# Performance work log

Measured on AMD Instinct MI355X. Metric: run time of the kernel, lower is better.

The kernel has to match this reference:

```python
import jax, jax.numpy as jnp
import numpy as np

E = 8      # n_rm_states
D = 256    # flattened input dim
H = 64     # hidden width (hard-coded in module)
A = 18     # n_actions
B = 65536  # batch


def setup_inputs() -> dict:
    key = jax.random.key(0)
    ks = jax.random.split(key, 16)
    s = lambda k, shape, fan_in: jax.random.normal(k, shape, jnp.float32) * (1.0 / np.sqrt(fan_in))
    inp = {
        "state": jax.random.normal(ks[0], (B, D), jnp.float32),
        "rm_state": jax.random.randint(ks[1], (B,), 0, E),
        # stacked per-expert params: layer i weight [E, in, out], bias [E, out]
        "W1": s(ks[2], (E, D, H), D), "b1": jnp.zeros((E, H), jnp.float32),
        "W2": s(ks[3], (E, H, H), H), "b2": jnp.zeros((E, H), jnp.float32),
        "W3": s(ks[4], (E, H, H), H), "b3": jnp.zeros((E, H), jnp.float32),
        "W4": s(ks[5], (E, H, H), H), "b4": jnp.zeros((E, H), jnp.float32),
        "W5": s(ks[6], (E, H, H), H), "b5": jnp.zeros((E, H), jnp.float32),
        "W6": s(ks[7], (E, H, A), H), "b6": jnp.zeros((E, A), jnp.float32),
    }
    return inp


def reference(state, rm_state, W1, b1, W2, b2, W3, b3, W4, b4, W5, b5, W6, b6):
    x = state.reshape(state.shape[0], -1)              # [B, D]
    # Run all E expert MLPs densely over the batch, then select per-row expert.
    h = jax.nn.relu(jnp.einsum('bd,edh->ebh', x, W1) + b1[:, None, :])   # [E, B, H]
    h = jax.nn.relu(jnp.einsum('ebh,ehk->ebk', h, W2) + b2[:, None, :])
    h = jax.nn.relu(jnp.einsum('ebh,ehk->ebk', h, W3) + b3[:, None, :])
    h = jax.nn.relu(jnp.einsum('ebh,ehk->ebk', h, W4) + b4[:, None, :])
    h = jax.nn.relu(jnp.einsum('ebh,ehk->ebk', h, W5) + b5[:, None, :])
    out_all = jnp.einsum('ebh,eha->eba', h, W6) + b6[:, None, :]          # [E, B, A]
    # scatter-back: actions[b] = expert[rm_state[b]](x[b])
    actions = out_all[rm_state, jnp.arange(x.shape[0])]                    # [B, A]
    return actions
```

## Files before the change

### kernel.cpp

```cpp
#include <hip/hip_runtime.h>


#define NE   8
#define DIM  256
#define HID  64
#define NA   18

typedef __attribute__((ext_vector_type(8))) short short8;
typedef __attribute__((ext_vector_type(4))) float f32x4;
#define MFMA __builtin_amdgcn_mfma_f32_16x16x32_bf16

__device__ __forceinline__ unsigned short f2bf(float f) {
    unsigned u = __builtin_bit_cast(unsigned, f);
    u += 0x7fff + ((u >> 16) & 1);
    return (unsigned short)(u >> 16);
}
__device__ __forceinline__ float bf2f(unsigned short h) {
    unsigned u = ((unsigned)h) << 16;
    return __builtin_bit_cast(float, u);
}
__device__ __forceinline__ void split8(const float* xs, short8& hi, short8& lo) {
    #pragma unroll
    for (int j = 0; j < 8; ++j) {
        unsigned short h = f2bf(xs[j]);
        hi[j] = (short)h;
        lo[j] = (short)f2bf(xs[j] - bf2f(h));
    }
}

__global__ __launch_bounds__(256) void histo_kernel(const int* __restrict__ rm,
                                                    int* __restrict__ hist) {
    __shared__ int wc[4][NE];
    const int t = threadIdx.x, w = t >> 6, l = t & 63;
    const int e = rm[blockIdx.x * 256 + t];
    #pragma unroll
    for (int q = 0; q < NE; ++q) {
        unsigned long long m = __ballot(e == q);
        if (l == 0) wc[w][q] = __popcll(m);
    }
    __syncthreads();
    if (t < NE) hist[blockIdx.x * NE + t] = wc[0][t] + wc[1][t] + wc[2][t] + wc[3][t];
}

__global__ __launch_bounds__(256) void scan_kernel(const int* __restrict__ hist,
                                                   int* __restrict__ base,
                                                   int* __restrict__ meta) {
    __shared__ int s[256][NE];
    __shared__ int tot[NE];
    const int t = threadIdx.x;
    int v[NE], own[NE];
    #pragma unroll
    for (int e = 0; e < NE; ++e) { own[e] = hist[t * NE + e]; v[e] = own[e]; }
    for (int off = 1; off < 256; off <<= 1) {
        #pragma unroll
        for (int e = 0; e < NE; ++e) s[t][e] = v[e];
        __syncthreads();
        if (t >= off) {
            #pragma unroll
            for (int e = 0; e < NE; ++e) v[e] += s[t - off][e];
        }
        __syncthreads();
    }
    if (t == 255) {
        #pragma unroll
        for (int e = 0; e < NE; ++e) tot[e] = v[e];
    }
    __syncthreads();
    int es[NE + 1]; es[0] = 0;
    #pragma unroll
    for (int e = 0; e < NE; ++e) es[e + 1] = es[e] + tot[e];
    #pragma unroll
    for (int e = 0; e < NE; ++e) base[t * NE + e] = es[e] + v[e] - own[e];
    if (t == 0) {
        #pragma unroll
        for (int e = 0; e < NE; ++e) meta[e] = tot[e];
        #pragma unroll
        for (int e = 0; e <= NE; ++e) meta[8 + e] = es[e];
        int ts = 0; meta[17] = 0;
        #pragma unroll
        for (int e = 0; e < NE; ++e) { ts += (tot[e] + 63) >> 6; meta[17 + e + 1] = ts; }
    }
}

__global__ __launch_bounds__(256) void scatter_kernel(const int* __restrict__ rm,
                                                      const int* __restrict__ base,
                                                      int* __restrict__ perm) {
    __shared__ int wc[4][NE];
    __shared__ int wb[4][NE];
    const int t = threadIdx.x, w = t >> 6, l = t & 63;
    const int i = blockIdx.x * 256 + t;
    const int e = rm[i];
    const unsigned long long ltm = (1ull << l) - 1ull;
    int rank = 0;
    #pragma unroll
    for (int q = 0; q < NE; ++q) {
        unsigned long long m = __ballot(e == q);
        if (e == q) rank = __popcll(m & ltm);
        if (l == 0) wc[w][q] = __popcll(m);
    }
    __syncthreads();
    if (t < 32) {
        int ww = t >> 3, q = t & 7;
        int b = base[blockIdx.x * NE + q];
        for (int p = 0; p < ww; ++p) b += wc[p][q];
        wb[ww][q] = b;
    }
    __syncthreads();
    perm[wb[w][e] + rank] = i;
}

__global__ __launch_bounds__(256) void prep_kernel(
    const float* __restrict__ W1, const float* __restrict__ W2,
    const float* __restrict__ W3, const float* __restrict__ W4,
    const float* __restrict__ W5, const float* __restrict__ W6,
    short* __restrict__ W1H, short* __restrict__ W1L,
    short* __restrict__ W2H, short* __restrict__ W2L,
    short* __restrict__ W3H, short* __restrict__ W3L,
    short* __restrict__ W4H, short* __restrict__ W4L,
    short* __restrict__ W5H, short* __restrict__ W5L,
    short* __restrict__ W6H, short* __restrict__ W6L) {
    const int idx = blockIdx.x * 256 + threadIdx.x;
    float v; short* H; short* L; int sidx;
    if (idx < 131072) {
        int e = idx >> 14, r = idx & 16383;
        int ks = r >> 11, nt = (r >> 9) & 3, l = (r >> 3) & 63, j = r & 7;
        int k = ks * 32 + ((l >> 4) << 3) + j, n = (nt << 4) + (l & 15);
        v = W1[(e * DIM + k) * HID + n];
        H = W1H; L = W1L; sidx = idx;
    } else if (idx < 131072 + 4 * 32768) {
        int layer = (idx - 131072) >> 15;
        int local = (idx - 131072) & 32767;
        int e = local >> 12, r = local & 4095;
        int ks = r >> 11, nt = (r >> 9) & 3, l = (r >> 3) & 63, j = r & 7;
        int k = ks * 32 + ((l >> 4) << 3) + j, n = (nt << 4) + (l & 15);
        const float* W = (layer == 0) ? W2 : (layer == 1) ? W3 : (layer == 2) ? W4 : W5;
        v = W[(e * HID + k) * HID + n];
        H = (layer == 0) ? W2H : (layer == 1) ? W3H : (layer == 2) ? W4H : W5H;
        L = (layer == 0) ? W2L : (layer == 1) ? W3L : (layer == 2) ? W4L : W5L;
        sidx = local;
    } else if (idx < 131072 + 4 * 32768 + 16384) {
        int local = idx - (131072 + 4 * 32768);
        int e = local >> 11, r = local & 2047;
        int ks = r >> 10, nt = (r >> 9) & 1, l = (r >> 3) & 63, j = r & 7;
        int k = ks * 32 + ((l >> 4) << 3) + j, n = (nt << 4) + (l & 15);
        v = (n < NA) ? W6[(e * HID + k) * NA + n] : 0.0f;
        H = W6H; L = W6L; sidx = local;
    } else return;
    unsigned short h = f2bf(v);
    H[sidx] = (short)h;
    L[sidx] = (short)f2bf(v - bf2f(h));
}

template <int NT>
__device__ __forceinline__ void gemm_k64(const float* hsrc, int l,
                                         const short* __restrict__ WH,
                                         const short* __restrict__ WL,
                                         f32x4* acc) {
    const int lg = l >> 4, lr = l & 15;
    #pragma unroll
    for (int ks = 0; ks < 2; ++ks) {
        const float* ap = hsrc + lr * 68 + ks * 32 + lg * 8;
        float4 v0 = *(const float4*)(ap);
        float4 v1 = *(const float4*)(ap + 4);
        float xs[8] = {v0.x, v0.y, v0.z, v0.w, v1.x, v1.y, v1.z, v1.w};
        short8 ahi, alo; split8(xs, ahi, alo);
        #pragma unroll
        for (int nt = 0; nt < NT; ++nt) {
            const short8 bhi = *(const short8*)(WH + ((ks * NT + nt) * 64 + l) * 8);
            const short8 blo = *(const short8*)(WL + ((ks * NT + nt) * 64 + l) * 8);
            acc[nt] = MFMA(ahi, bhi, acc[nt], 0, 0, 0);
            acc[nt] = MFMA(alo, bhi, acc[nt], 0, 0, 0);
            acc[nt] = MFMA(ahi, blo, acc[nt], 0, 0, 0);
        }
    }
}

template <int NT, bool RELU>
__device__ __forceinline__ void finish_to_lds(float* hdst, int l,
                                              const float* __restrict__ bias,
                                              f32x4* acc) {
    const int lg = l >> 4, lr = l & 15;
    #pragma unroll
    for (int nt = 0; nt < NT; ++nt) {
        float bv = bias[nt * 16 + lr];
        #pragma unroll
        for (int r = 0; r < 4; ++r) {
            float v = acc[nt][r] + bv;
            if (RELU) v = fmaxf(v, 0.0f);
            hdst[(lg * 4 + r) * 68 + nt * 16 + lr] = v;
        }
    }
}

__global__ __launch_bounds__(256) void mlp_mfma(
    const float* __restrict__ x, const int* __restrict__ perm,
    const int* __restrict__ meta,
    const short* __restrict__ W1H, const short* __restrict__ W1L,
    const short* __restrict__ W2H, const short* __restrict__ W2L,
    const short* __restrict__ W3H, const short* __restrict__ W3L,
    const short* __restrict__ W4H, const short* __restrict__ W4L,
    const short* __restrict__ W5H, const short* __restrict__ W5L,
    const short* __restrict__ W6H, const short* __restrict__ W6L,
    const float* __restrict__ b1, const float* __restrict__ b2,
    const float* __restrict__ b3, const float* __restrict__ b4,
    const float* __restrict__ b5, const float* __restrict__ b6,
    float* __restrict__ out) {
    __shared__ __align__(16) float hbuf[4][16][68];
    const int blk = blockIdx.x;
    if (blk >= meta[17 + NE]) return;
    int e = 0;
    #pragma unroll 1
    while (blk >= meta[17 + e + 1]) ++e;
    const int lt = blk - meta[17 + e];
    const int cnt = meta[e];
    const int pbase = meta[8 + e];
    const int t = threadIdx.x, w = t >> 6, l = t & 63;
    const int lg = l >> 4, lr = l & 15;
    const int li = lt * 64 + w * 16 + lr;
    const int row = perm[pbase + min(li, cnt - 1)];
    float* hw = &hbuf[w][0][0];
    const f32x4 zero = {0.0f, 0.0f, 0.0f, 0.0f};

    {
        f32x4 acc[4] = {zero, zero, zero, zero};
        const float* xr = x + (size_t)row * DIM + lg * 8;
        const short* WHp = W1H + (size_t)e * 32 * 512 + l * 8;
        const short* WLp = W1L + (size_t)e * 32 * 512 + l * 8;
        #pragma unroll
        for (int ks = 0; ks < 8; ++ks) {
            float4 v0 = *(const float4*)(xr + ks * 32);
            float4 v1 = *(const float4*)(xr + ks * 32 + 4);
            float xs[8] = {v0.x, v0.y, v0.z, v0.w, v1.x, v1.y, v1.z, v1.w};
            short8 ahi, alo; split8(xs, ahi, alo);
            #pragma unroll
            for (int nt = 0; nt < 4; ++nt) {
                const short8 bhi = *(const short8*)(WHp + (ks * 4 + nt) * 512);
                const short8 blo = *(const short8*)(WLp + (ks * 4 + nt) * 512);
                acc[nt] = MFMA(ahi, bhi, acc[nt], 0, 0, 0);
                acc[nt] = MFMA(alo, bhi, acc[nt], 0, 0, 0);
                acc[nt] = MFMA(ahi, blo, acc[nt], 0, 0, 0);
            }
        }
        finish_to_lds<4, true>(hw, l, b1 + e * HID, acc);
    }
    {
        f32x4 acc[4] = {zero, zero, zero, zero};
        gemm_k64<4>(hw, l, W2H + e * 8 * 512, W2L + e * 8 * 512, acc);
        finish_to_lds<4, true>(hw, l, b2 + e * HID, acc);
    }
    {
        f32x4 acc[4] = {zero, zero, zero, zero};
        gemm_k64<4>(hw, l, W3H + e * 8 * 512, W3L + e * 8 * 512, acc);
        finish_to_lds<4, true>(hw, l, b3 + e * HID, acc);
    }
    {
        f32x4 acc[4] = {zero, zero, zero, zero};
        gemm_k64<4>(hw, l, W4H + e * 8 * 512, W4L + e * 8 * 512, acc);
        finish_to_lds<4, true>(hw, l, b4 + e * HID, acc);
    }
    {
        f32x4 acc[4] = {zero, zero, zero, zero};
        gemm_k64<4>(hw, l, W5H + e * 8 * 512, W5L + e * 8 * 512, acc);
        finish_to_lds<4, true>(hw, l, b5 + e * HID, acc);
    }
    {
        f32x4 acc[2] = {zero, zero};
        gemm_k64<2>(hw, l, W6H + e * 4 * 512, W6L + e * 4 * 512, acc);
        const float* b6p = b6 + e * NA;
        #pragma unroll
        for (int r = 0; r < 4; ++r) {
            const int drow = lg * 4 + r;
            const int rs = __shfl(row, drow, 64);
            const bool valid = (lt * 64 + w * 16 + drow) < cnt;
            #pragma unroll
            for (int nt = 0; nt < 2; ++nt) {
                const int col = nt * 16 + lr;
                if (valid && col < NA)
                    out[(size_t)rs * NA + col] = acc[nt][r] + b6p[col];
            }
        }
    }
}

extern "C" void kernel_launch(void* const* d_in, const int* in_sizes, int n_in,
                              void* d_out, int out_size, void* d_ws, size_t ws_size,
                              hipStream_t stream) {
    const float* x  = (const float*)d_in[0];
    const int*   rm = (const int*)d_in[1];
    const float* W1 = (const float*)d_in[2];   const float* b1 = (const float*)d_in[3];
    const float* W2 = (const float*)d_in[4];   const float* b2 = (const float*)d_in[5];
    const float* W3 = (const float*)d_in[6];   const float* b3 = (const float*)d_in[7];
    const float* W4 = (const float*)d_in[8];   const float* b4 = (const float*)d_in[9];
    const float* W5 = (const float*)d_in[10];  const float* b5 = (const float*)d_in[11];
    const float* W6 = (const float*)d_in[12];  const float* b6 = (const float*)d_in[13];
    float* out = (float*)d_out;

    const int B = in_sizes[1];
    const int nblk = B / 256;

    int* hist = (int*)d_ws;
    int* base = hist + nblk * NE;
    int* meta = base + nblk * NE;
    int* perm = meta + 32;
    short* W1H = (short*)(perm + B);
    short* W1L = W1H + 131072;
    short* W2H = W1L + 131072;  short* W2L = W2H + 32768;
    short* W3H = W2L + 32768;   short* W3L = W3H + 32768;
    short* W4H = W3L + 32768;   short* W4L = W4H + 32768;
    short* W5H = W4L + 32768;   short* W5L = W5H + 32768;
    short* W6H = W5L + 32768;   short* W6L = W6H + 16384;

    histo_kernel<<<nblk, 256, 0, stream>>>(rm, hist);
    scan_kernel<<<1, 256, 0, stream>>>(hist, base, meta);
    scatter_kernel<<<nblk, 256, 0, stream>>>(rm, base, perm);
    prep_kernel<<<1088, 256, 0, stream>>>(W1, W2, W3, W4, W5, W6,
                                          W1H, W1L, W2H, W2L, W3H, W3L,
                                          W4H, W4L, W5H, W5L, W6H, W6L);
    mlp_mfma<<<B / 64 + NE, 256, 0, stream>>>(x, perm, meta,
                                              W1H, W1L, W2H, W2L, W3H, W3L,
                                              W4H, W4L, W5H, W5L, W6H, W6L,
                                              b1, b2, b3, b4, b5, b6, out);
}
```

Before: 153.9 us.

## Fuse prep/histogram and scan/scatter kernels; split MFMA accumulators into three chains

Merges the weight-split prep and the routing histogram into one launch, and merges the single-block scan with the scatter. Each scatter block now redoes the full 256-block scan redundantly using wave shuffles. This cuts four small launches plus the serial scan kernel down to two. In the MLP, the three bf16x3 MFMA products go into separate accumulators so they no longer form one dependent chain, B fragments are loaded before the MFMAs, packed bf16 conversion intrinsics are used, and launch bounds add an occupancy hint. These changes add register pressure and redundant scan work per block.

```diff
diff --git a/kernel.cpp b/kernel.cpp
--- a/kernel.cpp
+++ b/kernel.cpp
@@ -1,4 +1,5 @@
 #include <hip/hip_runtime.h>
+#include <hip/hip_bf16.h>
 
 
 #define NE   8
@@ -19,97 +20,26 @@
     unsigned u = ((unsigned)h) << 16;
     return __builtin_bit_cast(float, u);
 }
-__device__ __forceinline__ void split8(const float* xs, short8& hi, short8& lo) {
-    #pragma unroll
-    for (int j = 0; j < 8; ++j) {
-        unsigned short h = f2bf(xs[j]);
-        hi[j] = (short)h;
-        lo[j] = (short)f2bf(xs[j] - bf2f(h));
-    }
-}
-
-__global__ __launch_bounds__(256) void histo_kernel(const int* __restrict__ rm,
-                                                    int* __restrict__ hist) {
-    __shared__ int wc[4][NE];
-    const int t = threadIdx.x, w = t >> 6, l = t & 63;
-    const int e = rm[blockIdx.x * 256 + t];
-    #pragma unroll
-    for (int q = 0; q < NE; ++q) {
-        unsigned long long m = __ballot(e == q);
-        if (l == 0) wc[w][q] = __popcll(m);
-    }
-    __syncthreads();
-    if (t < NE) hist[blockIdx.x * NE + t] = wc[0][t] + wc[1][t] + wc[2][t] + wc[3][t];
-}
-
-__global__ __launch_bounds__(256) void scan_kernel(const int* __restrict__ hist,
-                                                   int* __restrict__ base,
-                                                   int* __restrict__ meta) {
-    __shared__ int s[256][NE];
-    __shared__ int tot[NE];
-    const int t = threadIdx.x;
-    int v[NE], own[NE];
-    #pragma unroll
-    for (int e = 0; e < NE; ++e) { own[e] = hist[t * NE + e]; v[e] = own[e]; }
-    for (int off = 1; off < 256; off <<= 1) {
-        #pragma unroll
-        for (int e = 0; e < NE; ++e) s[t][e] = v[e];
-        __syncthreads();
-        if (t >= off) {
-            #pragma unroll
-            for (int e = 0; e < NE; ++e) v[e] += s[t - off][e];
-        }
-        __syncthreads();
-    }
-    if (t == 255) {
-        #pragma unroll
-        for (int e = 0; e < NE; ++e) tot[e] = v[e];
-    }
-    __syncthreads();
-    int es[NE + 1]; es[0] = 0;
-    #pragma unroll
-    for (int e = 0; e < NE; ++e) es[e + 1] = es[e] + tot[e];
-    #pragma unroll
-    for (int e = 0; e < NE; ++e) base[t * NE + e] = es[e] + v[e] - own[e];
-    if (t == 0) {
-        #pragma unroll
-        for (int e = 0; e < NE; ++e) meta[e] = tot[e];
-        #pragma unroll
-        for (int e = 0; e <= NE; ++e) meta[8 + e] = es[e];
-        int ts = 0; meta[17] = 0;
-        #pragma unroll
-        for (int e = 0; e < NE; ++e) { ts += (tot[e] + 63) >> 6; meta[17 + e + 1] = ts; }
-    }
-}
-
-__global__ __launch_bounds__(256) void scatter_kernel(const int* __restrict__ rm,
-                                                      const int* __restrict__ base,
-                                                      int* __restrict__ perm) {
-    __shared__ int wc[4][NE];
-    __shared__ int wb[4][NE];
-    const int t = threadIdx.x, w = t >> 6, l = t & 63;
-    const int i = blockIdx.x * 256 + t;
-    const int e = rm[i];
-    const unsigned long long ltm = (1ull << l) - 1ull;
-    int rank = 0;
-    #pragma unroll
-    for (int q = 0; q < NE; ++q) {
-        unsigned long long m = __ballot(e == q);
-        if (e == q) rank = __popcll(m & ltm);
-        if (l == 0) wc[w][q] = __popcll(m);
-    }
-    __syncthreads();
-    if (t < 32) {
-        int ww = t >> 3, q = t & 7;
-        int b = base[blockIdx.x * NE + q];
-        for (int p = 0; p < ww; ++p) b += wc[p][q];
-        wb[ww][q] = b;
-    }
-    __syncthreads();
-    perm[wb[w][e] + rank] = i;
-}
-
-__global__ __launch_bounds__(256) void prep_kernel(
+__device__ __forceinline__ void split8v(const float* xs, short8& hi, short8& lo) {
+    float back[8];
+    #pragma unroll
+    for (int p = 0; p < 4; ++p) {
+        __hip_bfloat162 h2 = __float22bfloat162_rn(make_float2(xs[2*p], xs[2*p+1]));
+        hi[2*p]   = (short)__builtin_bit_cast(unsigned short, h2.x);
+        hi[2*p+1] = (short)__builtin_bit_cast(unsigned short, h2.y);
+        float2 b2 = __bfloat1622float2(h2);
+        back[2*p] = b2.x; back[2*p+1] = b2.y;
+    }
+    #pragma unroll
+    for (int p = 0; p < 4; ++p) {
+        __hip_bfloat162 l2 = __float22bfloat162_rn(
+            make_float2(xs[2*p] - back[2*p], xs[2*p+1] - back[2*p+1]));
+        lo[2*p]   = (short)__builtin_bit_cast(unsigned short, l2.x);
+        lo[2*p+1] = (short)__builtin_bit_cast(unsigned short, l2.y);
+    }
+}
+
+__global__ __launch_bounds__(256) void prep_histo(
     const float* __restrict__ W1, const float* __restrict__ W2,
     const float* __restrict__ W3, const float* __restrict__ W4,
     const float* __restrict__ W5, const float* __restrict__ W6,
@@ -118,8 +48,24 @@
     short* __restrict__ W3H, short* __restrict__ W3L,
     short* __restrict__ W4H, short* __restrict__ W4L,
     short* __restrict__ W5H, short* __restrict__ W5L,
-    short* __restrict__ W6H, short* __restrict__ W6L) {
-    const int idx = blockIdx.x * 256 + threadIdx.x;
+    short* __restrict__ W6H, short* __restrict__ W6L,
+    const int* __restrict__ rm, int* __restrict__ hist) {
+    const int bid = blockIdx.x;
+    if (bid >= 1088) {
+        __shared__ int wch[4][NE];
+        const int blk = bid - 1088;
+        const int t = threadIdx.x, w = t >> 6, l = t & 63;
+        const int e = rm[blk * 256 + t];
+        #pragma unroll
+        for (int q = 0; q < NE; ++q) {
+            unsigned long long m = __ballot(e == q);
+            if (l == 0) wch[w][q] = __popcll(m);
+        }
+        __syncthreads();
+        if (t < NE) hist[blk * NE + t] = wch[0][t] + wch[1][t] + wch[2][t] + wch[3][t];
+        return;
+    }
+    const int idx = bid * 256 + threadIdx.x;
     float v; short* H; short* L; int sidx;
     if (idx < 131072) {
         int e = idx >> 14, r = idx & 16383;
@@ -138,24 +84,90 @@
         H = (layer == 0) ? W2H : (layer == 1) ? W3H : (layer == 2) ? W4H : W5H;
         L = (layer == 0) ? W2L : (layer == 1) ? W3L : (layer == 2) ? W4L : W5L;
         sidx = local;
-    } else if (idx < 131072 + 4 * 32768 + 16384) {
+    } else {
         int local = idx - (131072 + 4 * 32768);
         int e = local >> 11, r = local & 2047;
         int ks = r >> 10, nt = (r >> 9) & 1, l = (r >> 3) & 63, j = r & 7;
         int k = ks * 32 + ((l >> 4) << 3) + j, n = (nt << 4) + (l & 15);
         v = (n < NA) ? W6[(e * HID + k) * NA + n] : 0.0f;
         H = W6H; L = W6L; sidx = local;
-    } else return;
+    }
     unsigned short h = f2bf(v);
     H[sidx] = (short)h;
     L[sidx] = (short)f2bf(v - bf2f(h));
+}
+
+__global__ __launch_bounds__(512) void scan_scatter(const int* __restrict__ rm,
+                                                    const int* __restrict__ hist,
+                                                    int* __restrict__ perm,
+                                                    int* __restrict__ meta) {
+    __shared__ int sbuf[NE][256];
+    __shared__ int wc[8][NE];
+    __shared__ int wb2[4][NE];
+    __shared__ int baseE[NE];
+    const int t = threadIdx.x, w = t >> 6, l = t & 63;
+    const int myblk = blockIdx.x;
+
+    {
+        int v0 = hist[(l * 4 + 0) * NE + w];
+        int v1 = hist[(l * 4 + 1) * NE + w];
+        int v2 = hist[(l * 4 + 2) * NE + w];
+        int v3 = hist[(l * 4 + 3) * NE + w];
+        v1 += v0; v2 += v1; v3 += v2;
+        int s = v3;
+        #pragma unroll
+        for (int off = 1; off < 64; off <<= 1) {
+            int u = __shfl_up(s, off);
+            if (l >= off) s += u;
+        }
+        const int ex = s - v3;
+        sbuf[w][l * 4 + 0] = ex + v0;
+        sbuf[w][l * 4 + 1] = ex + v1;
+        sbuf[w][l * 4 + 2] = ex + v2;
+        sbuf[w][l * 4 + 3] = ex + v3;
+    }
+    __syncthreads();
+    if (t < NE) {
+        int es = 0;
+        for (int q = 0; q < t; ++q) es += sbuf[q][255];
+        baseE[t] = es + (myblk ? sbuf[t][myblk - 1] : 0);
+    }
+    if (myblk == 0 && t == 0) {
+        int es = 0, ts = 0;
+        meta[8] = 0; meta[17] = 0;
+        for (int e = 0; e < NE; ++e) {
+            int c = sbuf[e][255];
+            meta[e] = c;
+            es += c; meta[8 + e + 1] = es;
+            ts += (c + 63) >> 6; meta[17 + e + 1] = ts;
+        }
+    }
+    const int i = myblk * 256 + t;
+    const int e_row = (t < 256) ? rm[i] : -1;
+    const unsigned long long ltm = (1ull << l) - 1ull;
+    int rank = 0;
+    #pragma unroll
+    for (int q = 0; q < NE; ++q) {
+        unsigned long long m = __ballot(e_row == q);
+        if (e_row == q) rank = __popcll(m & ltm);
+        if (l == 0) wc[w][q] = __popcll(m);
+    }
+    __syncthreads();
+    if (t < 32) {
+        int ww = t >> 3, q = t & 7;
+        int b = baseE[q];
+        for (int p = 0; p < ww; ++p) b += wc[p][q];
+        wb2[ww][q] = b;
+    }
+    __syncthreads();
+    if (t < 256) perm[wb2[w][e_row] + rank] = i;
 }
 
 template <int NT>
 __device__ __forceinline__ void gemm_k64(const float* hsrc, int l,
                                          const short* __restrict__ WH,
                                          const short* __restrict__ WL,
-                                         f32x4* acc) {
+                                         f32x4* a0, f32x4* a1, f32x4* a2) {
     const int lg = l >> 4, lr = l & 15;
     #pragma unroll
     for (int ks = 0; ks < 2; ++ks) {
@@ -163,14 +175,18 @@
         float4 v0 = *(const float4*)(ap);
         float4 v1 = *(const float4*)(ap + 4);
         float xs[8] = {v0.x, v0.y, v0.z, v0.w, v1.x, v1.y, v1.z, v1.w};
-        short8 ahi, alo; split8(xs, ahi, alo);
+        short8 ahi, alo; split8v(xs, ahi, alo);
+        short8 bh[NT], bl[NT];
         #pragma unroll
         for (int nt = 0; nt < NT; ++nt) {
-            const short8 bhi = *(const short8*)(WH + ((ks * NT + nt) * 64 + l) * 8);
-            const short8 blo = *(const short8*)(WL + ((ks * NT + nt) * 64 + l) * 8);
-            acc[nt] = MFMA(ahi, bhi, acc[nt], 0, 0, 0);
-            acc[nt] = MFMA(alo, bhi, acc[nt], 0, 0, 0);
-            acc[nt] = MFMA(ahi, blo, acc[nt], 0, 0, 0);
+            bh[nt] = *(const short8*)(WH + ((ks * NT + nt) * 64 + l) * 8);
+            bl[nt] = *(const short8*)(WL + ((ks * NT + nt) * 64 + l) * 8);
+        }
+        #pragma unroll
+        for (int nt = 0; nt < NT; ++nt) {
+            a0[nt] = MFMA(ahi, bh[nt], a0[nt], 0, 0, 0);
+            a1[nt] = MFMA(alo, bh[nt], a1[nt], 0, 0, 0);
+            a2[nt] = MFMA(ahi, bl[nt], a2[nt], 0, 0, 0);
         }
     }
 }
@@ -178,21 +194,21 @@
 template <int NT, bool RELU>
 __device__ __forceinline__ void finish_to_lds(float* hdst, int l,
                                               const float* __restrict__ bias,
-                                              f32x4* acc) {
+                                              f32x4* a0, f32x4* a1, f32x4* a2) {
     const int lg = l >> 4, lr = l & 15;
     #pragma unroll
     for (int nt = 0; nt < NT; ++nt) {
         float bv = bias[nt * 16 + lr];
         #pragma unroll
         for (int r = 0; r < 4; ++r) {
-            float v = acc[nt][r] + bv;
+            float v = (a0[nt][r] + a1[nt][r]) + (a2[nt][r] + bv);
             if (RELU) v = fmaxf(v, 0.0f);
             hdst[(lg * 4 + r) * 68 + nt * 16 + lr] = v;
         }
     }
 }
 
-__global__ __launch_bounds__(256) void mlp_mfma(
+__global__ __launch_bounds__(256, 4) void mlp_mfma(
     const float* __restrict__ x, const int* __restrict__ perm,
     const int* __restrict__ meta,
     const short* __restrict__ W1H, const short* __restrict__ W1L,
@@ -222,7 +238,9 @@
     const f32x4 zero = {0.0f, 0.0f, 0.0f, 0.0f};
 
     {
-        f32x4 acc[4] = {zero, zero, zero, zero};
+        f32x4 a0[4] = {zero, zero, zero, zero};
+        f32x4 a1[4] = {zero, zero, zero, zero};
+        f32x4 a2[4] = {zero, zero, zero, zero};
         const float* xr = x + (size_t)row * DIM + lg * 8;
         const short* WHp = W1H + (size_t)e * 32 * 512 + l * 8;
         const short* WLp = W1L + (size_t)e * 32 * 512 + l * 8;
@@ -231,41 +249,41 @@
             float4 v0 = *(const float4*)(xr + ks * 32);
             float4 v1 = *(const float4*)(xr + ks * 32 + 4);
             float xs[8] = {v0.x, v0.y, v0.z, v0.w, v1.x, v1.y, v1.z, v1.w};
-            short8 ahi, alo; split8(xs, ahi, alo);
+            short8 ahi, alo; split8v(xs, ahi, alo);
+            short8 bh[4], bl[4];
             #pragma unroll
             for (int nt = 0; nt < 4; ++nt) {
-                const short8 bhi = *(const short8*)(WHp + (ks * 4 + nt) * 512);
-                const short8 blo = *(const short8*)(WLp + (ks * 4 + nt) * 512);
-                acc[nt] = MFMA(ahi, bhi, acc[nt], 0, 0, 0);
-                acc[nt] = MFMA(alo, bhi, acc[nt], 0, 0, 0);
-                acc[nt] = MFMA(ahi, blo, acc[nt], 0, 0, 0);
+                bh[nt] = *(const short8*)(WHp + (ks * 4 + nt) * 512);
+                bl[nt] = *(const short8*)(WLp + (ks * 4 + nt) * 512);
             }
-        }
-        finish_to_lds<4, true>(hw, l, b1 + e * HID, acc);
-    }
+            #pragma unroll
+            for (int nt = 0; nt < 4; ++nt) {
+                a0[nt] = MFMA(ahi, bh[nt], a0[nt], 0, 0, 0);
+                a1[nt] = MFMA(alo, bh[nt], a1[nt], 0, 0, 0);
+                a2[nt] = MFMA(ahi, bl[nt], a2[nt], 0, 0, 0);
+            }
+        }
+        finish_to_lds<4, true>(hw, l, b1 + e * HID, a0, a1, a2);
+    }
+    #define HIDDEN(WH_, WL_, bias_)                                   \
+    {                                                                 \
+        f32x4 a0[4] = {zero, zero, zero, zero};                       \
+        f32x4 a1[4] = {zero, zero, zero, zero};                       \
+        f32x4 a2[4] = {zero, zero, zero, zero};                       \
+        gemm_k64<4>(hw, l, WH_ + e * 8 * 512, WL_ + e * 8 * 512,      \
+                    a0, a1, a2);                                      \
+        finish_to_lds<4, true>(hw, l, bias_ + e * HID, a0, a1, a2);   \
+    }
+    HIDDEN(W2H, W2L, b2)
+    HIDDEN(W3H, W3L, b3)
+    HIDDEN(W4H, W4L, b4)
+    HIDDEN(W5H, W5L, b5)
+    #undef HIDDEN
     {
-        f32x4 acc[4] = {zero, zero, zero, zero};
-        gemm_k64<4>(hw, l, W2H + e * 8 * 512, W2L + e * 8 * 512, acc);
-        finish_to_lds<4, true>(hw, l, b2 + e * HID, acc);
-    }
-    {
-        f32x4 acc[4] = {zero, zero, zero, zero};
-        gemm_k64<4>(hw, l, W3H + e * 8 * 512, W3L + e * 8 * 512, acc);
-        finish_to_lds<4, true>(hw, l, b3 + e * HID, acc);
-    }
-    {
-        f32x4 acc[4] = {zero, zero, zero, zero};
-        gemm_k64<4>(hw, l, W4H + e * 8 * 512, W4L + e * 8 * 512, acc);
-        finish_to_lds<4, true>(hw, l, b4 + e * HID, acc);
-    }
-    {
-        f32x4 acc[4] = {zero, zero, zero, zero};
-        gemm_k64<4>(hw, l, W5H + e * 8 * 512, W5L + e * 8 * 512, acc);
-        finish_to_lds<4, true>(hw, l, b5 + e * HID, acc);
-    }
-    {
-        f32x4 acc[2] = {zero, zero};
-        gemm_k64<2>(hw, l, W6H + e * 4 * 512, W6L + e * 4 * 512, acc);
+        f32x4 a0[2] = {zero, zero};
+        f32x4 a1[2] = {zero, zero};
+        f32x4 a2[2] = {zero, zero};
+        gemm_k64<2>(hw, l, W6H + e * 4 * 512, W6L + e * 4 * 512, a0, a1, a2);
         const float* b6p = b6 + e * NA;
         #pragma unroll
         for (int r = 0; r < 4; ++r) {
@@ -276,7 +294,7 @@
             for (int nt = 0; nt < 2; ++nt) {
                 const int col = nt * 16 + lr;
                 if (valid && col < NA)
-                    out[(size_t)rs * NA + col] = acc[nt][r] + b6p[col];
+                    out[(size_t)rs * NA + col] = (a0[nt][r] + a1[nt][r]) + (a2[nt][r] + b6p[col]);
             }
         }
     }
@@ -299,8 +317,7 @@
     const int nblk = B / 256;
 
     int* hist = (int*)d_ws;
-    int* base = hist + nblk * NE;
-    int* meta = base + nblk * NE;
+    int* meta = hist + nblk * NE;
     int* perm = meta + 32;
     short* W1H = (short*)(perm + B);
     short* W1L = W1H + 131072;
@@ -310,12 +327,11 @@
     short* W5H = W4L + 32768;   short* W5L = W5H + 32768;
     short* W6H = W5L + 32768;   short* W6L = W6H + 16384;
 
-    histo_kernel<<<nblk, 256, 0, stream>>>(rm, hist);
-    scan_kernel<<<1, 256, 0, stream>>>(hist, base, meta);
-    scatter_kernel<<<nblk, 256, 0, stream>>>(rm, base, perm);
-    prep_kernel<<<1088, 256, 0, stream>>>(W1, W2, W3, W4, W5, W6,
-                                          W1H, W1L, W2H, W2L, W3H, W3L,
-                                          W4H, W4L, W5H, W5L, W6H, W6L);
+    prep_histo<<<1088 + nblk, 256, 0, stream>>>(W1, W2, W3, W4, W5, W6,
+                                                W1H, W1L, W2H, W2L, W3H, W3L,
+                                                W4H, W4L, W5H, W5L, W6H, W6L,
+                                                rm, hist);
+    scan_scatter<<<nblk, 512, 0, stream>>>(rm, hist, perm, meta);
     mlp_mfma<<<B / 64 + NE, 256, 0, stream>>>(x, perm, meta,
                                               W1H, W1L, W2H, W2L, W3H, W3L,
                                               W4H, W4L, W5H, W5L, W6H, W6L,
```

Result: faster. 148.4 us (-3.6%).
